# Kernel optimization log

Hardware: AMD Instinct MI355X
Metric: run time of the kernel (lower is better)

## Reference

```python
import math
import jax, jax.numpy as jnp
from jax import lax
import numpy as np

N = 512          # transform size; frame size = 2N
B = 16           # batch
T = 2048         # number of frames; signal length = N*T
PI = math.pi


def _make_mdct_filter(n: int, normalize: bool = True) -> jnp.ndarray:
    # filter[k, 0, t] = cos(pi/N * (t + 0.5 + N/2) * (k + 0.5)) / sqrt(N)
    k = jnp.arange(n, dtype=jnp.float32).reshape(n, 1, 1)
    t = jnp.arange(2 * n, dtype=jnp.float32).reshape(1, 1, 2 * n)
    f = jnp.cos(PI / n * (t + 0.5 + n / 2) * (k + 0.5))
    if normalize:
        f = f / jnp.sqrt(jnp.float32(n))
    return f  # [N, 1, 2N]


def setup_inputs() -> dict:
    key = jax.random.key(0)
    x = jax.random.normal(key, (B, 1, N * T), dtype=jnp.float32)
    mdct_filter = _make_mdct_filter(N, normalize=True)
    return {"x": x, "mdct_filter": mdct_filter}


def reference(x, mdct_filter):
    # Equivalent of F.conv1d(x, filter, stride=N, padding=N)
    n = mdct_filter.shape[0]
    # x: [B, 1, N*T] -> out: [B, N, T+1]
    out = lax.conv_general_dilated(
        x, mdct_filter,
        window_strides=(n,),
        padding=[(n, n)],
        dimension_numbers=("NCH", "OIH", "NCH"),
    )
    return out
```

## Files before the change

### kernel.cpp

```cpp
#include <hip/hip_runtime.h>
#include <hip/hip_bf16.h>
#include <stdint.h>
#include <stddef.h>


constexpr int N_ = 512;
constexpr int T_ = 2048;
constexpr int B_ = 16;
constexpr int LEN = N_ * T_;
constexpr int FRAMES = T_ + 1;
constexpr int COLS = B_ * FRAMES;
constexpr int NT_TILES = 257;
constexpr int COLS_PAD = NT_TILES * 128;
constexpr int KF = 512;
constexpr int BK = 64;
constexpr int TILE_H = 128 * BK;

typedef __attribute__((ext_vector_type(8))) _Float16 f16x8;
typedef __attribute__((ext_vector_type(4))) _Float16 f16x4;
typedef __attribute__((ext_vector_type(4))) float f32x4;

#define GLD16(gptr, lptr)                                                     \
  __builtin_amdgcn_global_load_lds(                                           \
      (const __attribute__((address_space(1))) unsigned int*)(gptr),          \
      (__attribute__((address_space(3))) unsigned int*)(lptr), 16, 0, 0)

__global__ void prep_filter(const float* __restrict__ f,
                            _Float16* __restrict__ D) {
  int idx = (blockIdx.x * 256 + threadIdx.x) * 4;
  int k = idx >> 9;
  int j = idx & 511;
  int t = (j < 256) ? j : (j + 256);
  const float4 v = *(const float4*)&f[k * 1024 + t];
  f16x4 h = {(_Float16)v.x, (_Float16)v.y, (_Float16)v.z, (_Float16)v.w};
  *(f16x4*)&D[k * KF + j] = h;
}

__global__ void fold_x(const float* __restrict__ x, _Float16* __restrict__ V) {
  const int blk = (blockIdx.x & 7) * 1028 + (blockIdx.x >> 3);
  const int c = blk * 4 + (threadIdx.x >> 6);
  const int l = threadIdx.x & 63;
  const bool mi = (l < 32);
  const int j0 = mi ? (l * 8) : (256 + (l - 32) * 8);
  const float sgn = mi ? -1.0f : 1.0f;
  float4 a0 = {0.f, 0.f, 0.f, 0.f}, a1 = {0.f, 0.f, 0.f, 0.f};
  float4 r0 = {0.f, 0.f, 0.f, 0.f}, r1 = {0.f, 0.f, 0.f, 0.f};
  if (c < COLS) {
    int b = (int)((unsigned)c / (unsigned)FRAMES);
    int o = c - b * FRAMES;
    const int lo = b * LEN;
    const int g = lo + o * N_ - N_;
    const int fb = g + (mi ? j0 : (j0 + 256));
    const int rb = g + (mi ? (504 - j0) : (1272 - j0));
    if ((unsigned)(fb - lo) <= (unsigned)(LEN - 8)) {
      a0 = *(const float4*)(x + fb);
      a1 = *(const float4*)(x + fb + 4);
    }
    if ((unsigned)(rb - lo) <= (unsigned)(LEN - 8)) {
      r0 = *(const float4*)(x + rb);
      r1 = *(const float4*)(x + rb + 4);
    }
  }
  f16x8 h;
  h[0] = (_Float16)__builtin_fmaf(sgn, r1.w, a0.x);
  h[1] = (_Float16)__builtin_fmaf(sgn, r1.z, a0.y);
  h[2] = (_Float16)__builtin_fmaf(sgn, r1.y, a0.z);
  h[3] = (_Float16)__builtin_fmaf(sgn, r1.x, a0.w);
  h[4] = (_Float16)__builtin_fmaf(sgn, r0.w, a1.x);
  h[5] = (_Float16)__builtin_fmaf(sgn, r0.z, a1.y);
  h[6] = (_Float16)__builtin_fmaf(sgn, r0.y, a1.z);
  h[7] = (_Float16)__builtin_fmaf(sgn, r0.x, a1.w);
  if (c < COLS_PAD) *(f16x8*)&V[(size_t)c * KF + j0] = h;
}

__global__ __launch_bounds__(256, 2) void gemm_fold(
    const _Float16* __restrict__ D, const _Float16* __restrict__ V,
    float* __restrict__ out) {
  __shared__ __align__(16) _Float16 SMEM[4 * TILE_H];
  _Float16* const As0 = SMEM;
  _Float16* const Bs0 = SMEM + TILE_H;
  _Float16* const As1 = SMEM + 2 * TILE_H;
  _Float16* const Bs1 = SMEM + 3 * TILE_H;

  const int id = blockIdx.x;
  const int xcd = id & 7;
  const int sb = id >> 3;

  const int tid = threadIdx.x;
  const int wid = tid >> 6;
  const int lane = tid & 63;
  const int quad = lane >> 4;
  const int l16 = lane & 15;
  const int mw = (wid >> 1) * 64;
  const int nw = (wid & 1) * 64;

#define STAGE(AS, BS, KT)                                                     \
  do {                                                                        \
    const int kb_ = (KT) * BK;                                                \
    _Pragma("unroll")                                                         \
    for (int it = 0; it < 4; ++it) {                                          \
      const int S_ = it * 256 + tid;      \
      const int r_ = S_ >> 3;                                   \
      const int c_ = (S_ & 7) ^ (r_ & 7);          \
      const int g_ = kb_ + c_ * 8;                                            \
      GLD16(D + (size_t)(m0 + r_) * KF + g_, &(AS)[S_ * 8]);                  \
      GLD16(V + (size_t)(n0 + r_) * KF + g_, &(BS)[S_ * 8]);                  \
    }                                                                         \
  } while (0)

#define COMPUTE(AS, BS)                                                       \
  do {                                                                        \
    _Pragma("unroll")                                                         \
    for (int ko = 0; ko < 2; ++ko) {                                          \
      f16x8 af[4], bf[4];                                                     \
      _Pragma("unroll")                                                       \
      for (int i = 0; i < 4; ++i) {                                           \
        int ra_ = mw + i * 16 + l16;                                          \
        int rb_ = nw + i * 16 + l16;                                          \
        int ca_ = ko * 4 + quad;                                              \
        af[i] = *(const f16x8*)&(AS)[(ra_ * 8 + (ca_ ^ (ra_ & 7))) * 8];      \
        bf[i] = *(const f16x8*)&(BS)[(rb_ * 8 + (ca_ ^ (rb_ & 7))) * 8];      \
      }                                                                       \
      _Pragma("unroll")                                                       \
      for (int i = 0; i < 4; ++i)                                             \
        _Pragma("unroll")                                                     \
        for (int j = 0; j < 4; ++j)                                           \
          acc[i][j] = __builtin_amdgcn_mfma_f32_16x16x32_f16(af[i], bf[j],    \
                                                             acc[i][j],      \
                                                             0, 0, 0);        \
    }                                                                         \
  } while (0)

#define WAITV(N) asm volatile("s_waitcnt vmcnt(" #N ")" ::: "memory")
#define BAR() __builtin_amdgcn_s_barrier()
#define SCHED0() __builtin_amdgcn_sched_barrier(0)

#define STEP(AScur, BScur, ASnxt, BSnxt, KT)                                  \
  do {                                                                        \
    if ((KT) < 7) {                                                           \
      STAGE(ASnxt, BSnxt, (KT) + 1);                                          \
      WAITV(8);                                                               \
    } else {                                                                  \
      WAITV(0);                                                               \
    }                                                                         \
    BAR();                              \
    SCHED0();                                                                 \
    COMPUTE(AScur, BScur);                                                    \
    SCHED0();                                                                 \
    BAR();                     \
  } while (0)

  auto process = [&](int m0, int n0) {
    f32x4 acc[4][4];
#pragma unroll
    for (int i = 0; i < 4; ++i)
#pragma unroll
      for (int j = 0; j < 4; ++j) acc[i][j] = (f32x4){0.f, 0.f, 0.f, 0.f};

    STAGE(As0, Bs0, 0);

    STEP(As0, Bs0, As1, Bs1, 0);
    STEP(As1, Bs1, As0, Bs0, 1);
    STEP(As0, Bs0, As1, Bs1, 2);
    STEP(As1, Bs1, As0, Bs0, 3);
    STEP(As0, Bs0, As1, Bs1, 4);
    STEP(As1, Bs1, As0, Bs0, 5);
    STEP(As0, Bs0, As1, Bs1, 6);
    STEP(As1, Bs1, As0, Bs0, 7);

    const int bs = n0 / FRAMES;
    const int os = n0 - bs * FRAMES;
    const bool fast = (os + 128 <= FRAMES) && (n0 + 128 <= COLS);

    if (fast) {
      float* Ct = (float*)SMEM;
#pragma unroll
      for (int i = 0; i < 4; ++i) {
#pragma unroll
        for (int j = 0; j < 4; ++j) {
          const int Lr0 = mw + i * 16 + quad * 4;
          const int Lc = nw + j * 16 + l16;
#pragma unroll
          for (int r = 0; r < 4; ++r) {
            const int row = Lr0 + r;
            Ct[row * 128 + (Lc ^ ((row & 12) << 2))] = acc[i][j][r];
          }
        }
      }
      __syncthreads();
      float* const obase = out + (size_t)bs * N_ * FRAMES + os;
#pragma unroll 4
      for (int it2 = 0; it2 < 32; ++it2) {
        const int row = wid * 32 + it2;
        const int sw = (row & 12) << 2;
        const int grow = m0 + row;
        const float v0 = Ct[row * 128 + (lane ^ sw)];
        const float v1 = Ct[row * 128 + ((64 + lane) ^ sw)];
        float* rp = obase + (size_t)grow * FRAMES;
        rp[lane] = v0;
        rp[64 + lane] = v1;
      }
    } else {
#pragma unroll
      for (int i = 0; i < 4; ++i) {
#pragma unroll
        for (int j = 0; j < 4; ++j) {
          int col = n0 + nw + j * 16 + l16;
          if (col < COLS) {
            int b = col / FRAMES;
            int o = col - b * FRAMES;
            int rowb = m0 + mw + i * 16 + quad * 4;
            float* op = out + (size_t)b * N_ * FRAMES + (size_t)rowb * FRAMES + o;
#pragma unroll
            for (int r = 0; r < 4; ++r) op[(size_t)r * FRAMES] = acc[i][j][r];
          }
        }
      }
    }
  };

  process((sb & 3) * 128, ((sb >> 2) * 8 + xcd) * 128);

  if (id < 4) {
    BAR();
    process(id * 128, 256 * 128);
  }

#undef STEP
#undef STAGE
#undef COMPUTE
#undef WAITV
#undef BAR
#undef SCHED0
}

__global__ void naive_conv(const float* __restrict__ x, const float* __restrict__ f,
                           float* __restrict__ out) {
  int col = blockIdx.x;
  int k = threadIdx.x;
  __shared__ float win[1024];
  int b = col / FRAMES;
  int o = col - b * FRAMES;
  const float* xb = x + (size_t)b * LEN;
  int g = o * N_ - N_;
  for (int t = threadIdx.x; t < 1024; t += 512) {
    int i = g + t;
    win[t] = (i >= 0 && i < LEN) ? xb[i] : 0.0f;
  }
  __syncthreads();
  float s = 0.0f;
  const float* fk = f + (size_t)k * 1024;
  for (int t = 0; t < 1024; ++t) s += win[t] * fk[t];
  out[(size_t)b * N_ * FRAMES + (size_t)k * FRAMES + o] = s;
}

extern "C" void kernel_launch(void* const* d_in, const int* in_sizes, int n_in,
                              void* d_out, int out_size, void* d_ws, size_t ws_size,
                              hipStream_t stream) {
  const float* x = (const float*)d_in[0];
  const float* f = (const float*)d_in[1];
  float* out = (float*)d_out;

  const size_t elems_D = (size_t)512 * 512;
  const size_t elems_V = (size_t)COLS_PAD * KF;
  const size_t need = (elems_D + elems_V) * sizeof(_Float16);

  if (ws_size < need) {
    naive_conv<<<COLS, 512, 0, stream>>>(x, f, out);
    return;
  }

  _Float16* D = (_Float16*)d_ws;
  _Float16* V = D + elems_D;

  prep_filter<<<256, 256, 0, stream>>>(f, D);
  fold_x<<<COLS_PAD / 4, 256, 0, stream>>>(x, V);
  gemm_fold<<<1024, 256, 0, stream>>>(D, V, out);
}
```

Measured before the change: 142.6 us.

## Fuse input folding into GEMM staging, removing the separate fold kernel

```diff
diff --git a/kernel.cpp b/kernel.cpp
--- a/kernel.cpp
+++ b/kernel.cpp
@@ -36,45 +36,8 @@
   *(f16x4*)&D[k * KF + j] = h;
 }
 
-__global__ void fold_x(const float* __restrict__ x, _Float16* __restrict__ V) {
-  const int blk = (blockIdx.x & 7) * 1028 + (blockIdx.x >> 3);
-  const int c = blk * 4 + (threadIdx.x >> 6);
-  const int l = threadIdx.x & 63;
-  const bool mi = (l < 32);
-  const int j0 = mi ? (l * 8) : (256 + (l - 32) * 8);
-  const float sgn = mi ? -1.0f : 1.0f;
-  float4 a0 = {0.f, 0.f, 0.f, 0.f}, a1 = {0.f, 0.f, 0.f, 0.f};
-  float4 r0 = {0.f, 0.f, 0.f, 0.f}, r1 = {0.f, 0.f, 0.f, 0.f};
-  if (c < COLS) {
-    int b = (int)((unsigned)c / (unsigned)FRAMES);
-    int o = c - b * FRAMES;
-    const int lo = b * LEN;
-    const int g = lo + o * N_ - N_;
-    const int fb = g + (mi ? j0 : (j0 + 256));
-    const int rb = g + (mi ? (504 - j0) : (1272 - j0));
-    if ((unsigned)(fb - lo) <= (unsigned)(LEN - 8)) {
-      a0 = *(const float4*)(x + fb);
-      a1 = *(const float4*)(x + fb + 4);
-    }
-    if ((unsigned)(rb - lo) <= (unsigned)(LEN - 8)) {
-      r0 = *(const float4*)(x + rb);
-      r1 = *(const float4*)(x + rb + 4);
-    }
-  }
-  f16x8 h;
-  h[0] = (_Float16)__builtin_fmaf(sgn, r1.w, a0.x);
-  h[1] = (_Float16)__builtin_fmaf(sgn, r1.z, a0.y);
-  h[2] = (_Float16)__builtin_fmaf(sgn, r1.y, a0.z);
-  h[3] = (_Float16)__builtin_fmaf(sgn, r1.x, a0.w);
-  h[4] = (_Float16)__builtin_fmaf(sgn, r0.w, a1.x);
-  h[5] = (_Float16)__builtin_fmaf(sgn, r0.z, a1.y);
-  h[6] = (_Float16)__builtin_fmaf(sgn, r0.y, a1.z);
-  h[7] = (_Float16)__builtin_fmaf(sgn, r0.x, a1.w);
-  if (c < COLS_PAD) *(f16x8*)&V[(size_t)c * KF + j0] = h;
-}
-
 __global__ __launch_bounds__(256, 2) void gemm_fold(
-    const _Float16* __restrict__ D, const _Float16* __restrict__ V,
+    const float* __restrict__ x, const _Float16* __restrict__ D,
     float* __restrict__ out) {
   __shared__ __align__(16) _Float16 SMEM[4 * TILE_H];
   _Float16* const As0 = SMEM;
@@ -93,19 +56,69 @@
   const int l16 = lane & 15;
   const int mw = (wid >> 1) * 64;
   const int nw = (wid & 1) * 64;
-
-#define STAGE(AS, BS, KT)                                                     \
+  const int cl = tid >> 1;
+  const int h = tid & 1;
+
+#define WAITV(N) asm volatile("s_waitcnt vmcnt(" #N ")" ::: "memory")
+#define WAITLGKM() asm volatile("s_waitcnt lgkmcnt(0)" ::: "memory")
+#define BAR() __builtin_amdgcn_s_barrier()
+#define SCHED0() __builtin_amdgcn_sched_barrier(0)
+
+#define ASTAGE(AS, KT)                                                        \
   do {                                                                        \
     const int kb_ = (KT) * BK;                                                \
     _Pragma("unroll")                                                         \
     for (int it = 0; it < 4; ++it) {                                          \
-      const int S_ = it * 256 + tid;      \
-      const int r_ = S_ >> 3;                                   \
-      const int c_ = (S_ & 7) ^ (r_ & 7);          \
-      const int g_ = kb_ + c_ * 8;                                            \
-      GLD16(D + (size_t)(m0 + r_) * KF + g_, &(AS)[S_ * 8]);                  \
-      GLD16(V + (size_t)(n0 + r_) * KF + g_, &(BS)[S_ * 8]);                  \
-    }                                                                         \
+      const int S_ = it * 256 + tid;                                          \
+      const int r_ = S_ >> 3;                                                 \
+      const int c_ = (S_ & 7) ^ (r_ & 7);                                     \
+      GLD16(D + (size_t)(m0 + r_) * KF + kb_ + c_ * 8, &(AS)[S_ * 8]);        \
+    }                                                                         \
+  } while (0)
+
+#define XISSUE(KT)                                                            \
+  do {                                                                        \
+    const int kb_ = (KT) * BK;                                                \
+    const int fb_ = gg + ((kb_ < 256) ? (kb_ + 32 * h)                        \
+                                      : (kb_ + 256 + 32 * h));                \
+    const int rb_ = gg + ((kb_ < 256) ? (480 - kb_ - 32 * h)                  \
+                                      : (1248 - kb_ - 32 * h));               \
+    f0 = f1 = f2 = f3 = f4 = f5 = f6 = f7 = (float4){0.f, 0.f, 0.f, 0.f};     \
+    r0 = r1 = r2 = r3 = r4 = r5 = r6 = r7 = (float4){0.f, 0.f, 0.f, 0.f};     \
+    if (cok && (unsigned)(fb_ - lo) <= (unsigned)(LEN - 32)) {                \
+      const float4* p_ = (const float4*)(x + fb_);                            \
+      f0 = p_[0]; f1 = p_[1]; f2 = p_[2]; f3 = p_[3];                         \
+      f4 = p_[4]; f5 = p_[5]; f6 = p_[6]; f7 = p_[7];                         \
+    }                                                                         \
+    if (cok && (unsigned)(rb_ - lo) <= (unsigned)(LEN - 32)) {                \
+      const float4* q_ = (const float4*)(x + rb_);                            \
+      r0 = q_[0]; r1 = q_[1]; r2 = q_[2]; r3 = q_[3];                         \
+      r4 = q_[4]; r5 = q_[5]; r6 = q_[6]; r7 = q_[7];                         \
+    }                                                                         \
+  } while (0)
+
+#define FW8(BP, G8, A0, A1, R1, R0, SG)                                       \
+  do {                                                                        \
+    f16x8 hh_;                                                                \
+    hh_[0] = (_Float16)__builtin_fmaf(SG, (R1).w, (A0).x);                    \
+    hh_[1] = (_Float16)__builtin_fmaf(SG, (R1).z, (A0).y);                    \
+    hh_[2] = (_Float16)__builtin_fmaf(SG, (R1).y, (A0).z);                    \
+    hh_[3] = (_Float16)__builtin_fmaf(SG, (R1).x, (A0).w);                    \
+    hh_[4] = (_Float16)__builtin_fmaf(SG, (R0).w, (A1).x);                    \
+    hh_[5] = (_Float16)__builtin_fmaf(SG, (R0).z, (A1).y);                    \
+    hh_[6] = (_Float16)__builtin_fmaf(SG, (R0).y, (A1).z);                    \
+    hh_[7] = (_Float16)__builtin_fmaf(SG, (R0).x, (A1).w);                    \
+    const int sl_ = cl * 8 + ((4 * h + (G8)) ^ (cl & 7));                     \
+    *(f16x8*)&(BP)[sl_ * 8] = hh_;                                            \
+  } while (0)
+
+#define FOLD_WRITE(BS, KT)                                                    \
+  do {                                                                        \
+    const float sg_ = ((KT) * BK < 256) ? -1.0f : 1.0f;                       \
+    FW8((BS), 0, f0, f1, r7, r6, sg_);                                        \
+    FW8((BS), 1, f2, f3, r5, r4, sg_);                                        \
+    FW8((BS), 2, f4, f5, r3, r2, sg_);                                        \
+    FW8((BS), 3, f6, f7, r1, r0, sg_);                                        \
   } while (0)
 
 #define COMPUTE(AS, BS)                                                       \
@@ -131,33 +144,47 @@
     }                                                                         \
   } while (0)
 
-#define WAITV(N) asm volatile("s_waitcnt vmcnt(" #N ")" ::: "memory")
-#define BAR() __builtin_amdgcn_s_barrier()
-#define SCHED0() __builtin_amdgcn_sched_barrier(0)
-
-#define STEP(AScur, BScur, ASnxt, BSnxt, KT)                                  \
-  do {                                                                        \
+#define STEP(ASc, BSc, ASn, BSn, KT)                                          \
+  do {                                                                        \
+    if ((KT) < 7) ASTAGE(ASn, (KT) + 1);                                      \
+    SCHED0();                                                                 \
+    COMPUTE(ASc, BSc);                                                        \
+    SCHED0();                                                                 \
     if ((KT) < 7) {                                                           \
-      STAGE(ASnxt, BSnxt, (KT) + 1);                                          \
-      WAITV(8);                                                               \
-    } else {                                                                  \
-      WAITV(0);                                                               \
-    }                                                                         \
-    BAR();                              \
-    SCHED0();                                                                 \
-    COMPUTE(AScur, BScur);                                                    \
-    SCHED0();                                                                 \
-    BAR();                     \
+      WAITV(4);                   \
+      FOLD_WRITE(BSn, (KT) + 1);                                              \
+      if ((KT) < 6) XISSUE((KT) + 2);                                         \
+      WAITLGKM();                       \
+      if ((KT) < 6) { WAITV(16); } else { WAITV(0); }      \
+      BAR();                                                                  \
+    }                                                                         \
   } while (0)
 
   auto process = [&](int m0, int n0) {
+    const int c = n0 + cl;
+    const bool cok = (c < COLS);
+    const int b = (int)((unsigned)c / (unsigned)FRAMES);
+    const int o = c - b * FRAMES;
+    const int lo = b * LEN;
+    const int gg = lo + o * N_ - N_;
+
+    float4 f0, f1, f2, f3, f4, f5, f6, f7;
+    float4 r0, r1, r2, r3, r4, r5, r6, r7;
+
     f32x4 acc[4][4];
 #pragma unroll
     for (int i = 0; i < 4; ++i)
 #pragma unroll
       for (int j = 0; j < 4; ++j) acc[i][j] = (f32x4){0.f, 0.f, 0.f, 0.f};
 
-    STAGE(As0, Bs0, 0);
+    XISSUE(0);
+    ASTAGE(As0, 0);
+    WAITV(4);
+    FOLD_WRITE(Bs0, 0);
+    XISSUE(1);
+    WAITLGKM();
+    WAITV(16);
+    BAR();
 
     STEP(As0, Bs0, As1, Bs1, 0);
     STEP(As1, Bs1, As0, Bs0, 1);
@@ -167,6 +194,8 @@
     STEP(As1, Bs1, As0, Bs0, 5);
     STEP(As0, Bs0, As1, Bs1, 6);
     STEP(As1, Bs1, As0, Bs0, 7);
+
+    BAR();
 
     const int bs = n0 / FRAMES;
     const int os = n0 - bs * FRAMES;
@@ -207,10 +236,10 @@
         for (int j = 0; j < 4; ++j) {
           int col = n0 + nw + j * 16 + l16;
           if (col < COLS) {
-            int b = col / FRAMES;
-            int o = col - b * FRAMES;
+            int bb = col / FRAMES;
+            int oo = col - bb * FRAMES;
             int rowb = m0 + mw + i * 16 + quad * 4;
-            float* op = out + (size_t)b * N_ * FRAMES + (size_t)rowb * FRAMES + o;
+            float* op = out + (size_t)bb * N_ * FRAMES + (size_t)rowb * FRAMES + oo;
 #pragma unroll
             for (int r = 0; r < 4; ++r) op[(size_t)r * FRAMES] = acc[i][j][r];
           }
@@ -227,9 +256,13 @@
   }
 
 #undef STEP
-#undef STAGE
 #undef COMPUTE
+#undef FOLD_WRITE
+#undef FW8
+#undef XISSUE
+#undef ASTAGE
 #undef WAITV
+#undef WAITLGKM
 #undef BAR
 #undef SCHED0
 }
@@ -261,9 +294,7 @@
   const float* f = (const float*)d_in[1];
   float* out = (float*)d_out;
 
-  const size_t elems_D = (size_t)512 * 512;
-  const size_t elems_V = (size_t)COLS_PAD * KF;
-  const size_t need = (elems_D + elems_V) * sizeof(_Float16);
+  const size_t need = (size_t)512 * 512 * sizeof(_Float16);
 
   if (ws_size < need) {
     naive_conv<<<COLS, 512, 0, stream>>>(x, f, out);
@@ -271,9 +302,7 @@
   }
 
   _Float16* D = (_Float16*)d_ws;
-  _Float16* V = D + elems_D;
 
   prep_filter<<<256, 256, 0, stream>>>(f, D);
-  fold_x<<<COLS_PAD / 4, 256, 0, stream>>>(x, V);
-  gemm_fold<<<1024, 256, 0, stream>>>(D, V, out);
+  gemm_fold<<<1024, 256, 0, stream>>>(x, D, out);
 }
```

Result: slower. 180.5 us (+26.6%).
